# Performance work log

Hardware: AMD Instinct MI355X
Metric: run time of the kernel (lower is better)

Reference implementation:

```python
import jax, jax.numpy as jnp
import numpy as np

B, L, E, H = 8, 1024, 512, 8
E2 = 2 * E
EPS = 1e-5


def _spectral_fc(x, w, fw, fb, n):
    # rfft along feature dim, multiply by rfft of learned filter w (1,n), irfft back, then Linear
    xf = jnp.fft.rfft(x, axis=2, norm='ortho')          # [B,L,n//2+1] complex
    wf = jnp.fft.rfft(w, axis=1, norm='ortho')          # [1,n//2+1] complex
    y = jnp.fft.irfft(xf * wf, n=n, axis=2, norm='ortho')
    return y @ fw + fb


def _layernorm(x, g, b):
    m = jnp.mean(x, axis=-1, keepdims=True)
    v = jnp.mean(jnp.square(x - m), axis=-1, keepdims=True)
    return (x - m) * jax.lax.rsqrt(v + EPS) * g + b


def setup_inputs() -> dict:
    key = jax.random.key(0)
    ks = jax.random.split(key, 32)
    s = 0.02

    def lin_w(k, i, o):
        return (jax.random.normal(k, (i, o), jnp.float32) / np.sqrt(i)).astype(jnp.float32)

    def layer_params(k0, k1, n):
        return (s * jax.random.normal(k0, (1, n), jnp.float32), lin_w(k1, n, n), jnp.zeros((n,), jnp.float32))

    attn_w, attn_fw, attn_fb = layer_params(ks[1], ks[2], E)
    ln0_w, ln0_fw, ln0_fb = layer_params(ks[3], ks[4], E)
    ln1_w, ln1_fw, ln1_fb = layer_params(ks[5], ks[6], E)
    ln2_w, ln2_fw, ln2_fb = layer_params(ks[7], ks[8], E)
    ln3_w, ln3_fw, ln3_fb = layer_params(ks[9], ks[10], E2)
    ln4_w, ln4_fw, ln4_fb = layer_params(ks[11], ks[12], E2)

    return {
        'x': jax.random.normal(ks[0], (B, L, E), jnp.float32),
        'attn_w': attn_w, 'attn_fw': attn_fw, 'attn_fb': attn_fb,
        'ln0_w': ln0_w, 'ln0_fw': ln0_fw, 'ln0_fb': ln0_fb,
        'ln1_w': ln1_w, 'ln1_fw': ln1_fw, 'ln1_fb': ln1_fb,
        'ln2_w': ln2_w, 'ln2_fw': ln2_fw, 'ln2_fb': ln2_fb,
        'ln3_w': ln3_w, 'ln3_fw': ln3_fw, 'ln3_fb': ln3_fb,
        'ln4_w': ln4_w, 'ln4_fw': ln4_fw, 'ln4_fb': ln4_fb,
        'n1_g': jnp.ones((E,), jnp.float32), 'n1_b': jnp.zeros((E,), jnp.float32),
        'n2_g': jnp.ones((E,), jnp.float32), 'n2_b': jnp.zeros((E,), jnp.float32),
    }


def reference(x, attn_w, attn_fw, attn_fb,
              ln0_w, ln0_fw, ln0_fb, ln1_w, ln1_fw, ln1_fb,
              ln2_w, ln2_fw, ln2_fb, ln3_w, ln3_fw, ln3_fb,
              ln4_w, ln4_fw, ln4_fb, n1_g, n1_b, n2_g, n2_b):
    q = _spectral_fc(x, attn_w, attn_fw, attn_fb, E).reshape(B, L, H, E // H)
    scores = jnp.einsum('blhe,bshe->bhls', q, q) * (1.0 / np.sqrt(E))
    A = jax.nn.softmax(scores, axis=-1)
    new_x = jnp.einsum('bhls,bshd->blhd', A, q).reshape(B, L, E)

    x1 = _layernorm(x + new_x, n1_g, n1_b)
    x_ln = jax.nn.gelu(_spectral_fc(x1, ln0_w, ln0_fw, ln0_fb, E), approximate=False)
    x2 = x1 - x_ln
    h = jax.nn.sigmoid(_spectral_fc(x2, ln1_w, ln1_fw, ln1_fb, E)) * _spectral_fc(x2, ln2_w, ln2_fw, ln2_fb, E)
    out = jnp.concatenate((new_x, x_ln), axis=-1)  # [B,L,2E]
    out = jax.nn.sigmoid(_spectral_fc(out, ln3_w, ln3_fw, ln3_fb, E2)) * _spectral_fc(out, ln4_w, ln4_fw, ln4_fb, E2)
    return (_layernorm(h, n2_g, n2_b), out)
```

## Files before the change

### kernel.cpp

```cpp
#include <hip/hip_runtime.h>
#include <hip/hip_bf16.h>
#include <math.h>

typedef __hip_bfloat16 bf16;
typedef unsigned short u16;
typedef __attribute__((ext_vector_type(8))) short short8;
typedef __attribute__((ext_vector_type(4))) float f32x4;

#define NB      8
#define SEQ     1024
#define EDIM    512
#define E2DIM   1024
#define ROWS    8192
#define INV_SQRT_E 0.04419417382415922f
#define ATT_SCL    0.06375985678148161f

__device__ inline u16 f2bu(float f) {
    union { float f; unsigned u; } c; c.f = f;
    return (u16)((c.u + 0x7FFF + ((c.u >> 16) & 1)) >> 16);
}

__device__ __forceinline__ unsigned cvtpk_bf16(float lo, float hi) {
    unsigned r;
    asm("v_cvt_pk_bf16_f32 %0, %1, %2" : "=v"(r) : "v"(lo), "v"(hi));
    return r;
}

#define VMCNT(N) do { \
    asm volatile("s_waitcnt vmcnt(" #N ")" ::: "memory"); \
    __builtin_amdgcn_sched_barrier(0); \
    __builtin_amdgcn_s_barrier(); \
    __builtin_amdgcn_sched_barrier(0); } while (0)

#define LGKM0_BAR() do { \
    asm volatile("s_waitcnt lgkmcnt(0)" ::: "memory"); \
    __builtin_amdgcn_sched_barrier(0); \
    __builtin_amdgcn_s_barrier(); \
    __builtin_amdgcn_sched_barrier(0); } while (0)

__global__ __launch_bounds__(256) void detect_dtype(const u16* __restrict__ x,
                                                    int* __restrict__ flag) {
    int t = threadIdx.x;
    int cnt = 0;
    for (int k = t; k < 8192; k += 256) {
        int e = (x[k] >> 7) & 0xFF;
        if (e >= 0xC0) cnt++;
    }
#pragma unroll
    for (int o = 32; o > 0; o >>= 1) cnt += __shfl_xor(cnt, o);
    __shared__ int red[4];
    if ((t & 63) == 0) red[t >> 6] = cnt;
    __syncthreads();
    if (t == 0) flag[0] = (red[0] + red[1] + red[2] + red[3] > 100) ? 1 : 0;
}

struct CvtBatch {
    const void* src[23];
    float4*     dst[23];
    int         pre4[24];
};

__global__ __launch_bounds__(256) void cvt_all(CvtBatch a, int total4,
                                               const int* __restrict__ flag) {
    int t = blockIdx.x * 256 + threadIdx.x;
    if (t >= total4) return;
    int lo = 0;
    while (t >= a.pre4[lo + 1]) lo++;
    int li = t - a.pre4[lo];
    if (flag[0]) {
        a.dst[lo][li] = ((const float4*)a.src[lo])[li];
    } else {
        ushort4 u = ((const ushort4*)a.src[lo])[li];
        union { unsigned int i; float f; } c;
        float4 o;
        c.i = ((unsigned)u.x) << 16; o.x = c.f;
        c.i = ((unsigned)u.y) << 16; o.y = c.f;
        c.i = ((unsigned)u.z) << 16; o.z = c.f;
        c.i = ((unsigned)u.w) << 16; o.w = c.f;
        a.dst[lo][li] = o;
    }
}

__global__ __launch_bounds__(256) void f2b_kernel(const float* __restrict__ src,
                                                  u16* __restrict__ dst, int n4) {
    int i = blockIdx.x * 256 + threadIdx.x;
    if (i >= n4) return;
    float4 a = ((const float4*)src)[i];
    ushort4 o;
    o.x = f2bu(a.x); o.y = f2bu(a.y); o.z = f2bu(a.z); o.w = f2bu(a.w);
    ((ushort4*)dst)[i] = o;
}

#define LDK 32

__device__ __forceinline__ void stage128x32(const u16* g, int ld, u16* lds, int tid) {
    const int w = tid >> 6;
    const int l = tid & 63;
    const int r = w * 16 + (l >> 2);
    const int c = (l & 3) * 8;
    const u16* g0 = g + (size_t)r * ld + c;
    u16* l0 = lds + w * 16 * LDK;
    __builtin_amdgcn_global_load_lds(
        (const __attribute__((address_space(1))) void*)g0,
        (__attribute__((address_space(3))) void*)l0, 16, 0, 0);
    const u16* g1 = g0 + (size_t)64 * ld;
    u16* l1 = l0 + 64 * LDK;
    __builtin_amdgcn_global_load_lds(
        (const __attribute__((address_space(1))) void*)g1,
        (__attribute__((address_space(3))) void*)l1, 16, 0, 0);
}

__device__ __forceinline__ void stage64x32(const u16* g, int ld, u16* lds, int tid) {
    const int w = tid >> 6;
    const int l = tid & 63;
    const int r = w * 16 + (l >> 2);
    const int c = (l & 3) * 8;
    const u16* g0 = g + (size_t)r * ld + c;
    u16* l0 = lds + w * 16 * LDK;
    __builtin_amdgcn_global_load_lds(
        (const __attribute__((address_space(1))) void*)g0,
        (__attribute__((address_space(3))) void*)l0, 16, 0, 0);
}

__device__ __forceinline__ void stage64x64sw(const u16* g0, int ld, u16* lds,
                                             int wave, int lane) {
#pragma unroll
    for (int c = 0; c < 2; c++) {
        const int r  = wave * 16 + c * 8 + (lane >> 3);
        const int cg = (lane & 7) ^ (r & 7);
        const u16* g = g0 + (size_t)r * ld + cg * 8;
        u16* l = lds + (wave * 16 + c * 8) * 64;
        __builtin_amdgcn_global_load_lds(
            (const __attribute__((address_space(1))) void*)g,
            (__attribute__((address_space(3))) void*)l, 16, 0, 0);
    }
}

__device__ __forceinline__ void xcd_swz(int& bx, int& by) {
    const int nx  = gridDim.x;
    const int nwg = nx * gridDim.y;
    const int lid = blockIdx.y * nx + blockIdx.x;
    const int q   = nwg >> 3;
    const int s   = (lid & 7) * q + (lid >> 3);
    bx = s % nx;
    by = s / nx;
}

struct FoldBatch {
    const float* w[6];
    const float* fw[6];
    u16* t1[6];
    u16* t2[6];
    u16* mt[6];
    int  n[6], lg[6];
    float sc[6];
};

__global__ __launch_bounds__(256) void fold_trconv(FoldBatch fb) {
    const int z = blockIdx.z;
    const int n = fb.n[z];
    const int bx = blockIdx.x * 32, by = blockIdx.y * 32;
    if (bx >= n || by >= n) return;
    __shared__ float t[32][33];
    const int tx = threadIdx.x & 31, ty = threadIdx.x >> 5;
    const float* src = fb.fw[z];
    u16* dst = fb.t1[z];
#pragma unroll
    for (int r = 0; r < 32; r += 8)
        t[ty + r][tx] = src[(size_t)(by + ty + r) * n + bx + tx];
    __syncthreads();
#pragma unroll
    for (int r = 0; r < 32; r += 8)
        dst[(size_t)(bx + ty + r) * n + by + tx] = f2bu(t[tx][ty + r]);
}

__global__ __launch_bounds__(256) void fold_circ(FoldBatch fb) {
    const int z = blockIdx.z;
    const int n = fb.n[z], lg = fb.lg[z];
    int idx = blockIdx.x * 256 + threadIdx.x;
    if (idx >= n * n) return;
    int mask = n - 1;
    int m = idx & mask;
    int j = idx >> lg;
    fb.t2[z][idx] = f2bu(fb.w[z][(m - j) & mask]);
}

__global__ __launch_bounds__(256) void fold_gemm(FoldBatch fb) {
    const int z = blockIdx.z;
    const int n = fb.n[z];
    const int bm = blockIdx.y * 128, bn = blockIdx.x * 128;
    if (bm >= n || bn >= n) return;
    const u16* A  = fb.t1[z];
    const u16* Bt = fb.t2[z];
    u16* Mt = fb.mt[z];
    const float scale = fb.sc[z];

    __shared__ u16 Asl[2][128 * LDK];
    __shared__ u16 Bsl[2][128 * LDK];
    const int tid = threadIdx.x;
    const int lane = tid & 63, wave = tid >> 6;
    const int wy = wave >> 1, wx = wave & 1;
    const int qd = lane >> 4, ln16 = lane & 15;

    f32x4 acc[4][4];
#pragma unroll
    for (int i = 0; i < 4; i++)
#pragma unroll
        for (int j = 0; j < 4; j++)
#pragma unroll
            for (int r = 0; r < 4; r++) acc[i][j][r] = 0.f;

    const u16* Ab = A  + (size_t)bm * n;
    const u16* Bb = Bt + (size_t)bn * n;
    const int nt = n >> 5;
    stage128x32(Ab, n, Asl[0], tid);
    stage128x32(Bb, n, Bsl[0], tid);
    stage128x32(Ab + 32, n, Asl[1], tid);
    stage128x32(Bb + 32, n, Bsl[1], tid);
    int cur = 0;
    for (int t = 0; t < nt - 1; ++t) {
        VMCNT(4);
        const u16* Ac = Asl[cur];
        const u16* Bc = Bsl[cur];
        short8 af[4], bf_[4];
#pragma unroll
        for (int i = 0; i < 4; i++) {
            af[i]  = *(const short8*)&Ac[(wy * 64 + i * 16 + ln16) * LDK + qd * 8];
            bf_[i] = *(const short8*)&Bc[(wx * 64 + i * 16 + ln16) * LDK + qd * 8];
        }
        LGKM0_BAR();
        if (t + 2 < nt) {
            const int k2 = (t + 2) * 32;
            stage128x32(Ab + k2, n, Asl[cur], tid);
            stage128x32(Bb + k2, n, Bsl[cur], tid);
        }
#pragma unroll
        for (int i = 0; i < 4; i++)
#pragma unroll
            for (int j = 0; j < 4; j++)
                acc[i][j] = __builtin_amdgcn_mfma_f32_16x16x32_bf16(af[i], bf_[j], acc[i][j], 0, 0, 0);
        cur ^= 1;
    }
    VMCNT(0);
    {
        const u16* Ac = Asl[cur];
        const u16* Bc = Bsl[cur];
        short8 af[4], bf_[4];
#pragma unroll
        for (int i = 0; i < 4; i++) {
            af[i]  = *(const short8*)&Ac[(wy * 64 + i * 16 + ln16) * LDK + qd * 8];
            bf_[i] = *(const short8*)&Bc[(wx * 64 + i * 16 + ln16) * LDK + qd * 8];
        }
#pragma unroll
        for (int i = 0; i < 4; i++)
#pragma unroll
            for (int j = 0; j < 4; j++)
                acc[i][j] = __builtin_amdgcn_mfma_f32_16x16x32_bf16(af[i], bf_[j], acc[i][j], 0, 0, 0);
    }
#pragma unroll
    for (int i = 0; i < 4; i++)
#pragma unroll
        for (int j = 0; j < 4; j++) {
            const int col = bn + wx * 64 + j * 16 + ln16;
#pragma unroll
            for (int r = 0; r < 4; r++) {
                const int row = bm + wy * 64 + i * 16 + qd * 4 + r;
                Mt[(size_t)row * n + col] = f2bu(acc[i][j][r] * scale);
            }
        }
}

__global__ __launch_bounds__(256) void gemm_bf(
    const u16* __restrict__ A, int lda,
    const u16* __restrict__ Bt, int ldb,
    const float* __restrict__ bias,
    float* __restrict__ Cf, int ldc,
    u16* __restrict__ Cb, int ldcb,
    u16* __restrict__ Cb2, int ldcb2,
    const float* __restrict__ aux, int ldaux,
    int K, int mode)
{
    __shared__ u16 Asl[2][128 * LDK];
    __shared__ u16 Bsl[2][64 * LDK];
    const int tid = threadIdx.x;
    int bxs, bys;
    xcd_swz(bxs, bys);
    const int bm = bys * 128, bn = bxs * 64;
    const int lane = tid & 63, wave = tid >> 6;
    const int wy = wave >> 1, wx = wave & 1;
    const int qd = lane >> 4, ln16 = lane & 15;

    f32x4 acc[4][2];
#pragma unroll
    for (int i = 0; i < 4; i++)
#pragma unroll
        for (int j = 0; j < 2; j++)
#pragma unroll
            for (int r = 0; r < 4; r++) acc[i][j][r] = 0.f;

    const u16* Ab = A  + (size_t)bm * lda;
    const u16* Bb = Bt + (size_t)bn * ldb;
    const int nt = K >> 5;
    stage128x32(Ab, lda, Asl[0], tid);
    stage64x32(Bb, ldb, Bsl[0], tid);
    stage128x32(Ab + 32, lda, Asl[1], tid);
    stage64x32(Bb + 32, ldb, Bsl[1], tid);
    int cur = 0;
    for (int t = 0; t < nt - 1; ++t) {
        VMCNT(3);
        const u16* Ac = Asl[cur];
        const u16* Bc = Bsl[cur];
        short8 af[4], bf_[2];
#pragma unroll
        for (int i = 0; i < 4; i++)
            af[i]  = *(const short8*)&Ac[(wy * 64 + i * 16 + ln16) * LDK + qd * 8];
#pragma unroll
        for (int j = 0; j < 2; j++)
            bf_[j] = *(const short8*)&Bc[(wx * 32 + j * 16 + ln16) * LDK + qd * 8];
        LGKM0_BAR();
        if (t + 2 < nt) {
            const int k2 = (t + 2) * 32;
            stage128x32(Ab + k2, lda, Asl[cur], tid);
            stage64x32(Bb + k2, ldb, Bsl[cur], tid);
        }
#pragma unroll
        for (int i = 0; i < 4; i++)
#pragma unroll
            for (int j = 0; j < 2; j++)
                acc[i][j] = __builtin_amdgcn_mfma_f32_16x16x32_bf16(af[i], bf_[j], acc[i][j], 0, 0, 0);
        cur ^= 1;
    }
    VMCNT(0);
    {
        const u16* Ac = Asl[cur];
        const u16* Bc = Bsl[cur];
        short8 af[4], bf_[2];
#pragma unroll
        for (int i = 0; i < 4; i++)
            af[i]  = *(const short8*)&Ac[(wy * 64 + i * 16 + ln16) * LDK + qd * 8];
#pragma unroll
        for (int j = 0; j < 2; j++)
            bf_[j] = *(const short8*)&Bc[(wx * 32 + j * 16 + ln16) * LDK + qd * 8];
#pragma unroll
        for (int i = 0; i < 4; i++)
#pragma unroll
            for (int j = 0; j < 2; j++)
                acc[i][j] = __builtin_amdgcn_mfma_f32_16x16x32_bf16(af[i], bf_[j], acc[i][j], 0, 0, 0);
    }

#pragma unroll
    for (int i = 0; i < 4; i++) {
#pragma unroll
        for (int j = 0; j < 2; j++) {
            const int col = bn + wx * 32 + j * 16 + ln16;
            const float b_ = bias ? bias[col] : 0.f;
#pragma unroll
            for (int r = 0; r < 4; r++) {
                const int row = bm + wy * 64 + i * 16 + qd * 4 + r;
                float v = acc[i][j][r] + b_;
                if (mode == 1) v = 0.5f * v * (1.0f + erff(v * 0.7071067811865476f));
                if (Cf)  Cf[(size_t)row * ldc + col] = v;
                if (Cb)  Cb[(size_t)row * ldcb + col] = f2bu(v);
                if (Cb2) Cb2[(size_t)row * ldcb2 + col] =
                             f2bu(aux[(size_t)row * ldaux + col] - v);
            }
        }
    }
}

__global__ __launch_bounds__(256) void gemm_bf2(
    const u16* __restrict__ A, int lda,
    const u16* __restrict__ B1t, const u16* __restrict__ B2t, int ldb,
    const float* __restrict__ bias1, const float* __restrict__ bias2,
    float* __restrict__ Cf, int ldc, int K)
{
    __shared__ u16 Asl[2][128 * LDK];
    __shared__ u16 B1sl[2][64 * LDK];
    __shared__ u16 B2sl[2][64 * LDK];
    const int tid = threadIdx.x;
    int bxs, bys;
    xcd_swz(bxs, bys);
    const int bm = bys * 128, bn = bxs * 64;
    const int lane = tid & 63, wave = tid >> 6;
    const int wy = wave >> 1, wx = wave & 1;
    const int qd = lane >> 4, ln16 = lane & 15;

    f32x4 acc1[4][2], acc2[4][2];
#pragma unroll
    for (int i = 0; i < 4; i++)
#pragma unroll
        for (int j = 0; j < 2; j++)
#pragma unroll
            for (int r = 0; r < 4; r++) { acc1[i][j][r] = 0.f; acc2[i][j][r] = 0.f; }

    const u16* Ab  = A   + (size_t)bm * lda;
    const u16* B1b = B1t + (size_t)bn * ldb;
    const u16* B2b = B2t + (size_t)bn * ldb;
    const int nt = K >> 5;
    stage128x32(Ab,  lda, Asl[0],  tid);
    stage64x32(B1b, ldb, B1sl[0], tid);
    stage64x32(B2b, ldb, B2sl[0], tid);
    stage128x32(Ab + 32,  lda, Asl[1],  tid);
    stage64x32(B1b + 32, ldb, B1sl[1], tid);
    stage64x32(B2b + 32, ldb, B2sl[1], tid);
    int cur = 0;
    for (int t = 0; t < nt - 1; ++t) {
        VMCNT(4);
        const u16* Ac  = Asl[cur];
        const u16* B1c = B1sl[cur];
        const u16* B2c = B2sl[cur];
        short8 af[4], b1f[2], b2f[2];
#pragma unroll
        for (int i = 0; i < 4; i++)
            af[i]  = *(const short8*)&Ac [(wy * 64 + i * 16 + ln16) * LDK + qd * 8];
#pragma unroll
        for (int j = 0; j < 2; j++) {
            b1f[j] = *(const short8*)&B1c[(wx * 32 + j * 16 + ln16) * LDK + qd * 8];
            b2f[j] = *(const short8*)&B2c[(wx * 32 + j * 16 + ln16) * LDK + qd * 8];
        }
        LGKM0_BAR();
        if (t + 2 < nt) {
            const int k2 = (t + 2) * 32;
            stage128x32(Ab  + k2, lda, Asl[cur],  tid);
            stage64x32(B1b + k2, ldb, B1sl[cur], tid);
            stage64x32(B2b + k2, ldb, B2sl[cur], tid);
        }
#pragma unroll
        for (int i = 0; i < 4; i++)
#pragma unroll
            for (int j = 0; j < 2; j++) {
                acc1[i][j] = __builtin_amdgcn_mfma_f32_16x16x32_bf16(af[i], b1f[j], acc1[i][j], 0, 0, 0);
                acc2[i][j] = __builtin_amdgcn_mfma_f32_16x16x32_bf16(af[i], b2f[j], acc2[i][j], 0, 0, 0);
            }
        cur ^= 1;
    }
    VMCNT(0);
    {
        const u16* Ac  = Asl[cur];
        const u16* B1c = B1sl[cur];
        const u16* B2c = B2sl[cur];
        short8 af[4], b1f[2], b2f[2];
#pragma unroll
        for (int i = 0; i < 4; i++)
            af[i]  = *(const short8*)&Ac [(wy * 64 + i * 16 + ln16) * LDK + qd * 8];
#pragma unroll
        for (int j = 0; j < 2; j++) {
            b1f[j] = *(const short8*)&B1c[(wx * 32 + j * 16 + ln16) * LDK + qd * 8];
            b2f[j] = *(const short8*)&B2c[(wx * 32 + j * 16 + ln16) * LDK + qd * 8];
        }
#pragma unroll
        for (int i = 0; i < 4; i++)
#pragma unroll
            for (int j = 0; j < 2; j++) {
                acc1[i][j] = __builtin_amdgcn_mfma_f32_16x16x32_bf16(af[i], b1f[j], acc1[i][j], 0, 0, 0);
                acc2[i][j] = __builtin_amdgcn_mfma_f32_16x16x32_bf16(af[i], b2f[j], acc2[i][j], 0, 0, 0);
            }
    }

#pragma unroll
    for (int i = 0; i < 4; i++) {
#pragma unroll
        for (int j = 0; j < 2; j++) {
            const int col = bn + wx * 32 + j * 16 + ln16;
            const float b1_ = bias1[col], b2_ = bias2[col];
#pragma unroll
            for (int r = 0; r < 4; r++) {
                const int row = bm + wy * 64 + i * 16 + qd * 4 + r;
                const float g = 1.0f / (1.0f + expf(-(acc1[i][j][r] + b1_)));
                Cf[(size_t)row * ldc + col] = g * (acc2[i][j][r] + b2_);
            }
        }
    }
}

__global__ __launch_bounds__(256) void ln_kernel(
    const float* __restrict__ in0, int ld0,
    const u16* __restrict__ in1b, int ld1b,
    const float* __restrict__ g, const float* __restrict__ bta,
    float* __restrict__ outf, int ldo,
    u16* __restrict__ outb, int ldob)
{
    int row = blockIdx.x, tid = threadIdx.x;
    const float* p0 = in0 + (size_t)row * ld0;
    float v0 = p0[tid], v1 = p0[tid + 256];
    if (in1b) {
        const u16* p1 = in1b + (size_t)row * ld1b;
        union { unsigned u; float f; } c0, c1;
        c0.u = ((unsigned)p1[tid]) << 16;
        c1.u = ((unsigned)p1[tid + 256]) << 16;
        v0 += c0.f; v1 += c1.f;
    }
    float s = v0 + v1, sq = v0 * v0 + v1 * v1;
#pragma unroll
    for (int o = 32; o > 0; o >>= 1) {
        s  += __shfl_xor(s, o);
        sq += __shfl_xor(sq, o);
    }
    __shared__ float red[8];
    int wid = tid >> 6;
    if ((tid & 63) == 0) { red[wid] = s; red[4 + wid] = sq; }
    __syncthreads();
    s  = red[0] + red[1] + red[2] + red[3];
    sq = red[4] + red[5] + red[6] + red[7];
    float mean = s * (1.0f / 512.0f);
    float var  = sq * (1.0f / 512.0f) - mean * mean;
    float rstd = rsqrtf(var + 1e-5f);
    float o0 = (v0 - mean) * rstd * g[tid] + bta[tid];
    float o1 = (v1 - mean) * rstd * g[tid + 256] + bta[tid + 256];
    if (outf) {
        outf[(size_t)row * ldo + tid]       = o0;
        outf[(size_t)row * ldo + tid + 256] = o1;
    }
    if (outb) {
        outb[(size_t)row * ldob + tid]       = f2bu(o0);
        outb[(size_t)row * ldob + tid + 256] = f2bu(o1);
    }
}

__global__ __launch_bounds__(256) void trans_vt(const u16* __restrict__ q,
                                                u16* __restrict__ vt) {
    const int z  = blockIdx.z;
    const int bb = z >> 3, hh = z & 7;
    const int k0 = blockIdx.x * 64;
    const int d0 = blockIdx.y * 32;
    __shared__ u16 t[64][33];
    const int tx = threadIdx.x & 31, ty = threadIdx.x >> 5;
    const u16* src = q + (size_t)(bb * SEQ + k0) * EDIM + hh * 64 + d0;
#pragma unroll
    for (int r = 0; r < 64; r += 8)
        t[ty + r][tx] = src[(size_t)(ty + r) * EDIM + tx];
    __syncthreads();
    const int ox = threadIdx.x & 63, oy = threadIdx.x >> 6;
    u16* dst = vt + ((size_t)z * 64 + d0) * SEQ + k0;
#pragma unroll
    for (int r = 0; r < 32; r += 4)
        dst[(size_t)(oy + r) * SEQ + ox] = t[ox][oy + r];
}

#define AP 80
#define ANT 16

__global__ __launch_bounds__(256) void attn_mfma(const u16* __restrict__ qall,
                                                 const u16* __restrict__ vt,
                                                 u16* __restrict__ catb) {
    __shared__ u16 Ks2[2][64 * 64];
    __shared__ u16 VTs2[2][64 * 64];
    __shared__ u16 Pw[4][16 * AP];

    const int bid = blockIdx.x;
    const int lt = bid & 15, hh = (bid >> 4) & 7, bb = bid >> 7;
    const int q0 = lt * 64;
    const int tid = threadIdx.x;
    const int wave = tid >> 6, lane = tid & 63;
    const int quad = lane >> 4, ln16 = lane & 15;

    const u16* qh = qall + (size_t)bb * SEQ * EDIM + hh * 64;
    const u16* vh = vt + (size_t)(bb * 8 + hh) * 64 * SEQ;

    const u16* qrow = qh + (size_t)(q0 + wave * 16 + ln16) * EDIM + quad * 8;
    const short8 aq0 = *(const short8*)(qrow);
    const short8 aq1 = *(const short8*)(qrow + 32);

    f32x4 oacc[4];
    float m_run = -1e30f, l_run = 0.f;
#pragma unroll
    for (int j = 0; j < 4; j++)
#pragma unroll
        for (int r = 0; r < 4; r++) oacc[j][r] = 0.f;

    stage64x64sw(qh, EDIM, Ks2[0], wave, lane);
    stage64x64sw(vh, SEQ, VTs2[0], wave, lane);
    stage64x64sw(qh + (size_t)64 * EDIM, EDIM, Ks2[1], wave, lane);
    stage64x64sw(vh + 64, SEQ, VTs2[1], wave, lane);

    const int sw = ln16 & 7;
    const int c0 = (quad ^ sw) * 8;
    const int c1 = ((quad + 4) ^ sw) * 8;

    int cur = 0;
    for (int t = 0; t < ANT; ++t) {
        if (t < ANT - 1) { VMCNT(4); } else { VMCNT(0); }
        const u16* Kc = Ks2[cur];
        const u16* Vc = VTs2[cur];

        f32x4 S[4];
#pragma unroll
        for (int j = 0; j < 4; j++) {
            const int ro = (j * 16 + ln16) * 64;
            short8 a0 = *(const short8*)&Kc[ro + c0];
            short8 a1 = *(const short8*)&Kc[ro + c1];
            f32x4 c = {0.f, 0.f, 0.f, 0.f};
            c = __builtin_amdgcn_mfma_f32_16x16x32_bf16(a0, aq0, c, 0, 0, 0);
            c = __builtin_amdgcn_mfma_f32_16x16x32_bf16(a1, aq1, c, 0, 0, 0);
            S[j] = c;
        }

        float mx = S[0][0];
#pragma unroll
        for (int j = 0; j < 4; j++)
#pragma unroll
            for (int r = 0; r < 4; r++) mx = fmaxf(mx, S[j][r]);
        mx = fmaxf(mx, __shfl_xor(mx, 16));
        mx = fmaxf(mx, __shfl_xor(mx, 32));
        const float mn = fmaxf(m_run, mx);
        const float al = exp2f((m_run - mn) * ATT_SCL);
        m_run = mn;
        const float ns = -mn * ATT_SCL;
        float p[4][4];
        float rs = 0.f;
#pragma unroll
        for (int j = 0; j < 4; j++)
#pragma unroll
            for (int r = 0; r < 4; r++) {
                p[j][r] = exp2f(fmaf(S[j][r], ATT_SCL, ns));
                rs += p[j][r];
            }
        rs += __shfl_xor(rs, 16);
        rs += __shfl_xor(rs, 32);
        l_run = l_run * al + rs;

#pragma unroll
        for (int j = 0; j < 4; j++) {
            unsigned w0 = cvtpk_bf16(p[j][0], p[j][1]);
            unsigned w1 = cvtpk_bf16(p[j][2], p[j][3]);
            *(uint2*)&Pw[wave][ln16 * AP + j * 16 + quad * 4] = make_uint2(w0, w1);
        }

        float alq[4];
#pragma unroll
        for (int r = 0; r < 4; r++) alq[r] = __shfl(al, quad * 4 + r);
#pragma unroll
        for (int j = 0; j < 4; j++)
#pragma unroll
            for (int r = 0; r < 4; r++) oacc[j][r] *= alq[r];

        short8 pa0 = *(const short8*)&Pw[wave][ln16 * AP + quad * 8];
        short8 pa1 = *(const short8*)&Pw[wave][ln16 * AP + 32 + quad * 8];
        short8 vb0[4], vb1[4];
#pragma unroll
        for (int j = 0; j < 4; j++) {
            const int ro = (j * 16 + ln16) * 64;
            vb0[j] = *(const short8*)&Vc[ro + c0];
            vb1[j] = *(const short8*)&Vc[ro + c1];
        }

        LGKM0_BAR();
        if (t + 2 < ANT) {
            stage64x64sw(qh + (size_t)(t + 2) * 64 * EDIM, EDIM, Ks2[cur], wave, lane);
            stage64x64sw(vh + (t + 2) * 64, SEQ, VTs2[cur], wave, lane);
        }

#pragma unroll
        for (int j = 0; j < 4; j++) {
            oacc[j] = __builtin_amdgcn_mfma_f32_16x16x32_bf16(pa0, vb0[j], oacc[j], 0, 0, 0);
            oacc[j] = __builtin_amdgcn_mfma_f32_16x16x32_bf16(pa1, vb1[j], oacc[j], 0, 0, 0);
        }
        cur ^= 1;
    }

    const float linv = 1.0f / l_run;
    float invq[4];
#pragma unroll
    for (int r = 0; r < 4; r++) invq[r] = __shfl(linv, quad * 4 + r);
#pragma unroll
    for (int r = 0; r < 4; r++) {
        const int row = bb * SEQ + q0 + wave * 16 + quad * 4 + r;
#pragma unroll
        for (int j = 0; j < 4; j++) {
            const int col = hh * 64 + j * 16 + ln16;
            catb[(size_t)row * E2DIM + col] = f2bu(oacc[j][r] * invq[r]);
        }
    }
}

extern "C" void kernel_launch(void* const* d_in, const int* in_sizes, int n_in,
                              void* d_out, int out_size, void* d_ws, size_t ws_size,
                              hipStream_t stream)
{
    const size_t OFF_MT0 = 0;
    const size_t OFF_MT1 = OFF_MT0 + 131072;
    const size_t OFF_MT2 = OFF_MT1 + 131072;
    const size_t OFF_MT3 = OFF_MT2 + 131072;
    const size_t OFF_MT4 = OFF_MT3 + 131072;
    const size_t OFF_MT5 = OFF_MT4 + 524288;
    const size_t OFF_XB  = OFF_MT5 + 524288;
    const size_t OFF_CB  = OFF_XB + 2097152;
    const size_t OFF_BQ  = OFF_CB + 4194304;
    const size_t OFF_BN  = OFF_BQ + 4194304;
    const size_t OFF_BC  = OFF_BN + 4194304;
    const size_t OFF_P   = OFF_BC + 4194304;

    float* W = (float*)d_ws;
    u16* MT[6] = {(u16*)(W + OFF_MT0), (u16*)(W + OFF_MT1), (u16*)(W + OFF_MT2),
                  (u16*)(W + OFF_MT3), (u16*)(W + OFF_MT4), (u16*)(W + OFF_MT5)};
    u16*   XB  = (u16*)(W + OFF_XB);
    u16*   CB  = (u16*)(W + OFF_CB);
    u16*   QB  = (u16*)(W + OFF_BQ);
    float* BN  = W + OFF_BN;
    float* BC  = W + OFF_BC;
    u16*   VT  = (u16*)BN;

    float* F[23];
    CvtBatch cb;
    int pre = 0;
    for (int i = 0; i < 23 && i < n_in; i++) {
        cb.pre4[i] = pre;
        F[i] = W + OFF_P + (size_t)pre * 4;
        cb.src[i] = d_in[i];
        cb.dst[i] = (float4*)F[i];
        pre += in_sizes[i] / 4;
    }
    cb.pre4[23] = pre;
    const int total4 = pre;
    int* FLAG = (int*)(W + OFF_P + (size_t)total4 * 4);

    if (n_in < 23) return;
    if (ws_size < (OFF_P + (size_t)total4 * 4 + 16) * sizeof(float)) return;

    detect_dtype<<<1, 256, 0, stream>>>((const u16*)d_in[0], FLAG);
    cvt_all<<<(total4 + 255) / 256, 256, 0, stream>>>(cb, total4, FLAG);
    f2b_kernel<<<(ROWS * EDIM / 4 + 255) / 256, 256, 0, stream>>>(F[0], XB, ROWS * EDIM / 4);

    FoldBatch fb;
    {
        const int wi[6] = {1, 4, 7, 10, 13, 16};
        u16* T1 = (u16*)BN;
        u16* T2 = (u16*)BC;
        size_t off = 0;
        for (int s = 0; s < 6; s++) {
            const int n = (s < 4) ? 512 : 1024;
            fb.w[s]  = F[wi[s]];
            fb.fw[s] = F[wi[s] + 1];
            fb.t1[s] = T1 + off;
            fb.t2[s] = T2 + off;
            fb.mt[s] = MT[s];
            fb.n[s]  = n;
            fb.lg[s] = (s < 4) ? 9 : 10;
            fb.sc[s] = (s < 4) ? 0.04419417382415922f : 0.03125f;
            off += (size_t)n * n;
        }
    }
    fold_trconv<<<dim3(32, 32, 6), 256, 0, stream>>>(fb);
    fold_circ<<<dim3(4096, 1, 6), 256, 0, stream>>>(fb);
    fold_gemm<<<dim3(8, 8, 6), 256, 0, stream>>>(fb);

    float* out0 = (float*)d_out;
    float* out1 = (float*)d_out + (size_t)ROWS * EDIM;

    gemm_bf<<<dim3(8, 64), 256, 0, stream>>>(
        XB, 512, MT[0], 512, F[3], nullptr, 0, QB, 512, nullptr, 0, nullptr, 0, 512, 0);
    trans_vt<<<dim3(16, 2, 64), 256, 0, stream>>>(QB, VT);
    attn_mfma<<<1024, 256, 0, stream>>>(QB, VT, CB);
    ln_kernel<<<8192, 256, 0, stream>>>(F[0], 512, CB, 1024, F[19], F[20],
                                        BC, 512, XB, 512);
    gemm_bf<<<dim3(8, 64), 256, 0, stream>>>(
        XB, 512, MT[1], 512, F[6], nullptr, 0, CB + 512, 1024, QB, 512, BC, 512, 512, 1);
    gemm_bf2<<<dim3(8, 64), 256, 0, stream>>>(
        QB, 512, MT[2], MT[3], 512, F[9], F[12], BN, 512, 512);
    ln_kernel<<<8192, 256, 0, stream>>>(BN, 512, nullptr, 0, F[21], F[22],
                                        out0, 512, nullptr, 0);
    gemm_bf2<<<dim3(16, 64), 256, 0, stream>>>(
        CB, 1024, MT[4], MT[5], 1024, F[15], F[18], out1, 1024, 1024);
}
```

Baseline: 347.1 us.

## Single-buffer attention K/V staging and remap block order across batches

Replaces the double-buffered K/V LDS pipeline in the attention kernel with single buffers loaded synchronously each tile, bracketed by barriers. It also remaps blockIdx so consecutive physical blocks interleave across batches. The aim is to cut LDS usage and improve occupancy, and possibly cache locality across compute dies. In exchange, global-load latency is no longer overlapped with MFMA work.

```diff
diff --git a/kernel.cpp b/kernel.cpp
--- a/kernel.cpp
+++ b/kernel.cpp
@@ -543,11 +543,12 @@
 __global__ __launch_bounds__(256) void attn_mfma(const u16* __restrict__ qall,
                                                  const u16* __restrict__ vt,
                                                  u16* __restrict__ catb) {
-    __shared__ u16 Ks2[2][64 * 64];
-    __shared__ u16 VTs2[2][64 * 64];
+    __shared__ u16 Ks[64 * 64];
+    __shared__ u16 VTs[64 * 64];
     __shared__ u16 Pw[4][16 * AP];
 
-    const int bid = blockIdx.x;
+    const int phys = blockIdx.x;
+    const int bid = (phys & 7) * 128 + (phys >> 3);
     const int lt = bid & 15, hh = (bid >> 4) & 7, bb = bid >> 7;
     const int q0 = lt * 64;
     const int tid = threadIdx.x;
@@ -568,27 +569,22 @@
 #pragma unroll
         for (int r = 0; r < 4; r++) oacc[j][r] = 0.f;
 
-    stage64x64sw(qh, EDIM, Ks2[0], wave, lane);
-    stage64x64sw(vh, SEQ, VTs2[0], wave, lane);
-    stage64x64sw(qh + (size_t)64 * EDIM, EDIM, Ks2[1], wave, lane);
-    stage64x64sw(vh + 64, SEQ, VTs2[1], wave, lane);
-
     const int sw = ln16 & 7;
     const int c0 = (quad ^ sw) * 8;
     const int c1 = ((quad + 4) ^ sw) * 8;
 
-    int cur = 0;
     for (int t = 0; t < ANT; ++t) {
-        if (t < ANT - 1) { VMCNT(4); } else { VMCNT(0); }
-        const u16* Kc = Ks2[cur];
-        const u16* Vc = VTs2[cur];
+        if (t) __syncthreads();
+        stage64x64sw(qh + (size_t)t * 64 * EDIM, EDIM, Ks, wave, lane);
+        stage64x64sw(vh + t * 64, SEQ, VTs, wave, lane);
+        __syncthreads();
 
         f32x4 S[4];
 #pragma unroll
         for (int j = 0; j < 4; j++) {
             const int ro = (j * 16 + ln16) * 64;
-            short8 a0 = *(const short8*)&Kc[ro + c0];
-            short8 a1 = *(const short8*)&Kc[ro + c1];
+            short8 a0 = *(const short8*)&Ks[ro + c0];
+            short8 a1 = *(const short8*)&Ks[ro + c1];
             f32x4 c = {0.f, 0.f, 0.f, 0.f};
             c = __builtin_amdgcn_mfma_f32_16x16x32_bf16(a0, aq0, c, 0, 0, 0);
             c = __builtin_amdgcn_mfma_f32_16x16x32_bf16(a1, aq1, c, 0, 0, 0);
@@ -636,26 +632,14 @@
 
         short8 pa0 = *(const short8*)&Pw[wave][ln16 * AP + quad * 8];
         short8 pa1 = *(const short8*)&Pw[wave][ln16 * AP + 32 + quad * 8];
-        short8 vb0[4], vb1[4];
 #pragma unroll
         for (int j = 0; j < 4; j++) {
             const int ro = (j * 16 + ln16) * 64;
-            vb0[j] = *(const short8*)&Vc[ro + c0];
-            vb1[j] = *(const short8*)&Vc[ro + c1];
-        }
-
-        LGKM0_BAR();
-        if (t + 2 < ANT) {
-            stage64x64sw(qh + (size_t)(t + 2) * 64 * EDIM, EDIM, Ks2[cur], wave, lane);
-            stage64x64sw(vh + (t + 2) * 64, SEQ, VTs2[cur], wave, lane);
-        }
-
-#pragma unroll
-        for (int j = 0; j < 4; j++) {
-            oacc[j] = __builtin_amdgcn_mfma_f32_16x16x32_bf16(pa0, vb0[j], oacc[j], 0, 0, 0);
-            oacc[j] = __builtin_amdgcn_mfma_f32_16x16x32_bf16(pa1, vb1[j], oacc[j], 0, 0, 0);
-        }
-        cur ^= 1;
+            short8 b0 = *(const short8*)&VTs[ro + c0];
+            short8 b1 = *(const short8*)&VTs[ro + c1];
+            oacc[j] = __builtin_amdgcn_mfma_f32_16x16x32_bf16(pa0, b0, oacc[j], 0, 0, 0);
+            oacc[j] = __builtin_amdgcn_mfma_f32_16x16x32_bf16(pa1, b1, oacc[j], 0, 0, 0);
+        }
     }
 
     const float linv = 1.0f / l_run;
```

Measured after the change: 337.6 us. 2.7% less time.
